# Optimization experiments

Hardware: AMD Instinct MI355X
Metric: run time of the kernel (lower is better)

## Reference

```python
import jax, jax.numpy as jnp
import numpy as np

B, IN_DIM, OUT_DIM, N, H = 64, 2, 1, 512, 64
SEQ, HOR, K, NSUP = 12, 12, 2, 2
TOT = 1 + NSUP * K  # number of diffusion matrices (identity + K steps per support)


def _lin_init(key, fan_in, shape):
    return jax.random.normal(key, shape, jnp.float32) / np.sqrt(fan_in)


def setup_inputs() -> dict:
    key = jax.random.key(0)
    ks = jax.random.split(key, 16)
    inputs = jax.random.normal(ks[0], (B, IN_DIM, N, SEQ), jnp.float32)
    A = jax.random.uniform(ks[1], (NSUP, N, N), jnp.float32)
    supports = A / A.sum(axis=2, keepdims=True)  # row-normalized transition matrices
    params = {}
    i = 2
    for pre, in0 in (('e', IN_DIM), ('d', OUT_DIM)):
        for l in range(2):
            cin = (in0 if l == 0 else H) + H
            params[f'{pre}{l}_wg'] = _lin_init(ks[i], TOT * cin, (TOT * cin, 2 * H)); i += 1
            params[f'{pre}{l}_bg'] = jnp.zeros((2 * H,), jnp.float32)
            params[f'{pre}{l}_wc'] = _lin_init(ks[i], TOT * cin, (TOT * cin, H)); i += 1
            params[f'{pre}{l}_bc'] = jnp.zeros((H,), jnp.float32)
    params['proj_w'] = _lin_init(ks[i], H, (OUT_DIM, H))
    params['proj_b'] = jnp.zeros((OUT_DIM,), jnp.float32)
    return {'inputs': inputs, 'supports': supports, **params}


def _gconv(x, h, supports, W, b):
    # x: (B,Cx,N), h: (B,H,N) -> (B,Dout,N)
    z = jnp.concatenate([x, h], axis=1)
    feats = [z]
    for s in range(NSUP):
        xk = z
        for _ in range(K):
            xk = jnp.einsum('nm,bcm->bcn', supports[s], xk)
            feats.append(xk)
    zf = jnp.concatenate(feats, axis=1)  # (B, TOT*C, N)
    return jnp.einsum('bcn,cd->bdn', zf, W) + b[None, :, None]


def _cell(x, h, supports, wg, bg, wc, bc):
    ru = jax.nn.sigmoid(_gconv(x, h, supports, wg, bg))
    r, u = jnp.split(ru, 2, axis=1)
    c = jnp.tanh(_gconv(x, r * h, supports, wc, bc))
    return u * h + (1.0 - u) * c


def _run(inputs, supports, p):
    h0 = jnp.zeros((B, H, N), jnp.float32)
    h1 = jnp.zeros((B, H, N), jnp.float32)

    def enc_step(carry, x):
        h0, h1 = carry
        h0 = _cell(x, h0, supports, p['e0_wg'], p['e0_bg'], p['e0_wc'], p['e0_bc'])
        h1 = _cell(h0, h1, supports, p['e1_wg'], p['e1_bg'], p['e1_wc'], p['e1_bc'])
        return (h0, h1), None

    xs = jnp.moveaxis(inputs, -1, 0)  # (SEQ,B,IN_DIM,N)
    (h0, h1), _ = jax.lax.scan(enc_step, (h0, h1), xs)

    go = jnp.zeros((B, OUT_DIM, N), jnp.float32)

    def dec_step(carry, _):
        x, h0, h1 = carry
        h0 = _cell(x, h0, supports, p['d0_wg'], p['d0_bg'], p['d0_wc'], p['d0_bc'])
        h1 = _cell(h0, h1, supports, p['d1_wg'], p['d1_bg'], p['d1_wc'], p['d1_bc'])
        y = jnp.einsum('bhn,oh->bon', h1, p['proj_w']) + p['proj_b'][None, :, None]
        return (y, h0, h1), y

    _, ys = jax.lax.scan(dec_step, (go, h0, h1), None, length=HOR)
    return jnp.moveaxis(ys, 0, -1)  # (B, OUT_DIM, N, HOR)


def reference(inputs, supports, e0_wg, e0_bg, e0_wc, e0_bc, e1_wg, e1_bg, e1_wc, e1_bc,
              d0_wg, d0_bg, d0_wc, d0_bc, d1_wg, d1_bg, d1_wc, d1_bc, proj_w, proj_b):
    p = dict(e0_wg=e0_wg, e0_bg=e0_bg, e0_wc=e0_wc, e0_bc=e0_bc,
             e1_wg=e1_wg, e1_bg=e1_bg, e1_wc=e1_wc, e1_bc=e1_bc,
             d0_wg=d0_wg, d0_bg=d0_bg, d0_wc=d0_wc, d0_bc=d0_bc,
             d1_wg=d1_wg, d1_bg=d1_bg, d1_wc=d1_wc, d1_bc=d1_bc,
             proj_w=proj_w, proj_b=proj_b)
    return _run(inputs, supports, p)
```

## Files before the change

kernel.cpp:

```cpp
#include <hip/hip_runtime.h>

#define B_ 64
#define N_ 512

typedef __attribute__((ext_vector_type(8))) short bf8_t;
typedef __attribute__((ext_vector_type(16))) float f16_t;
typedef __attribute__((ext_vector_type(4))) float f4v_t;

#define MFMA32(a, b, c) __builtin_amdgcn_mfma_f32_32x32x16_bf16(a, b, c, 0, 0, 0)

__device__ __forceinline__ ushort f2bf(float x) {
  union { float f; unsigned u; } v; v.f = x;
  unsigned r = v.u + 0x7FFFu + ((v.u >> 16) & 1u);
  return (ushort)(r >> 16);
}
__device__ __forceinline__ float bf2f(ushort h) {
  union { unsigned u; float f; } v; v.u = ((unsigned)h) << 16;
  return v.f;
}

__device__ __forceinline__ void gld16(const ushort* g, ushort* l) {
  __builtin_amdgcn_global_load_lds(
      (const __attribute__((address_space(1))) unsigned int*)(uintptr_t)g,
      (__attribute__((address_space(3))) unsigned int*)(uintptr_t)l,
      16, 0, 0);
}

__device__ __forceinline__ int xcd_logical(int nwg) {
  int lin = blockIdx.x + gridDim.x * (blockIdx.y + gridDim.y * blockIdx.z);
  return (lin & 7) * (nwg >> 3) + (lin >> 3);
}

__device__ __forceinline__ int swz32(int r) { return (r >> 1) & 3; }

template <int ROWS, int THREADS>
__device__ __forceinline__ void stage_tile2(const ushort* g, int lda, int k0,
                                            ushort* l, int tid) {
  constexpr int RT = (ROWS * 32) / (THREADS * 8);
#pragma unroll
  for (int q = 0; q < RT; ++q) {
    int e  = q * THREADS * 8 + tid * 8;
    int r  = e >> 5;
    int c8 = (e >> 3) & 3;
    int g8 = c8 ^ swz32(r);
    gld16(g + (size_t)r * lda + k0 + g8 * 8, l + e);
  }
}

__device__ __forceinline__ void core128(
    const ushort* Ah, const ushort* Al, int lda,
    const ushort* Bh, const ushort* Bl, int ldb,
    int K, ushort* lds, f16_t acc[2][2]) {
  constexpr int TILE = 128 * 32;
  constexpr int SSZ  = 4 * TILE;
  const int tid = threadIdx.x, lane = tid & 63, wave = tid >> 6;
  const int ar = lane & 31, hb = lane >> 5;
  const int wm = wave >> 1, wn = wave & 1;

  auto stage = [&](int buf, int k0) {
    ushort* lb = lds + buf * SSZ;
    stage_tile2<128, 256>(Ah, lda, k0, lb, tid);
    stage_tile2<128, 256>(Al, lda, k0, lb + TILE, tid);
    stage_tile2<128, 256>(Bh, ldb, k0, lb + 2 * TILE, tid);
    stage_tile2<128, 256>(Bl, ldb, k0, lb + 3 * TILE, tid);
  };

  const int nc = K >> 5;
  stage(0, 0);
  int buf = 0;
  for (int c = 0; c < nc; ++c) {
    __syncthreads();
    if (c + 1 < nc) stage(buf ^ 1, (c + 1) << 5);
    const ushort* lb = lds + buf * SSZ;
#pragma unroll
    for (int ks = 0; ks < 2; ++ks) {
      bf8_t ah[2], al[2], bh[2], bl[2];
#pragma unroll
      for (int i = 0; i < 2; ++i) {
        int r = wm * 64 + 32 * i + ar;
        int c8 = (ks * 2 + hb) ^ swz32(r);
        ah[i] = *(const bf8_t*)(lb + r * 32 + c8 * 8);
        al[i] = *(const bf8_t*)(lb + TILE + r * 32 + c8 * 8);
      }
#pragma unroll
      for (int j = 0; j < 2; ++j) {
        int r = wn * 64 + 32 * j + ar;
        int c8 = (ks * 2 + hb) ^ swz32(r);
        bh[j] = *(const bf8_t*)(lb + 2 * TILE + r * 32 + c8 * 8);
        bl[j] = *(const bf8_t*)(lb + 3 * TILE + r * 32 + c8 * 8);
      }
#pragma unroll
      for (int i = 0; i < 2; ++i)
#pragma unroll
        for (int j = 0; j < 2; ++j) {
          acc[i][j] = MFMA32(ah[i], bh[j], acc[i][j]);
          acc[i][j] = MFMA32(ah[i], bl[j], acc[i][j]);
          acc[i][j] = MFMA32(al[i], bh[j], acc[i][j]);
        }
    }
    buf ^= 1;
  }
}

__device__ __forceinline__ void core128_1(
    const ushort* Ah, int lda,
    const ushort* Bh, int ldb,
    int K, ushort* lds, f16_t acc[2][2]) {
  constexpr int TILE = 128 * 32;
  constexpr int SSZ  = 2 * TILE;
  const int tid = threadIdx.x, lane = tid & 63, wave = tid >> 6;
  const int ar = lane & 31, hb = lane >> 5;
  const int wm = wave >> 1, wn = wave & 1;

  auto stage = [&](int buf, int k0) {
    ushort* lb = lds + buf * SSZ;
    stage_tile2<128, 256>(Ah, lda, k0, lb, tid);
    stage_tile2<128, 256>(Bh, ldb, k0, lb + TILE, tid);
  };

  const int nc = K >> 5;
  stage(0, 0);
  int buf = 0;
  for (int c = 0; c < nc; ++c) {
    __syncthreads();
    if (c + 1 < nc) stage(buf ^ 1, (c + 1) << 5);
    const ushort* lb = lds + buf * SSZ;
#pragma unroll
    for (int ks = 0; ks < 2; ++ks) {
      bf8_t ah[2], bh[2];
#pragma unroll
      for (int i = 0; i < 2; ++i) {
        int r = wm * 64 + 32 * i + ar;
        int c8 = (ks * 2 + hb) ^ swz32(r);
        ah[i] = *(const bf8_t*)(lb + r * 32 + c8 * 8);
      }
#pragma unroll
      for (int j = 0; j < 2; ++j) {
        int r = wn * 64 + 32 * j + ar;
        int c8 = (ks * 2 + hb) ^ swz32(r);
        bh[j] = *(const bf8_t*)(lb + TILE + r * 32 + c8 * 8);
      }
#pragma unroll
      for (int i = 0; i < 2; ++i)
#pragma unroll
        for (int j = 0; j < 2; ++j)
          acc[i][j] = MFMA32(ah[i], bh[j], acc[i][j]);
    }
    buf ^= 1;
  }
}

__device__ __forceinline__ int crow32(int r, int hb) {
  return (r & 3) + 8 * (r >> 2) + 4 * hb;
}

__global__ __launch_bounds__(256) void ssq_k(const float* __restrict__ S,
                                             float* __restrict__ SS) {
  int s = blockIdx.z;
  const float* Ss = S + s * N_ * N_;
  __shared__ float Ta[16][17], Tb[16][17];
  int n = blockIdx.y * 16 + threadIdx.y;
  int m = blockIdx.x * 16 + threadIdx.x;
  float acc = 0.f;
  for (int p0 = 0; p0 < N_; p0 += 16) {
    Ta[threadIdx.y][threadIdx.x] = Ss[n * N_ + p0 + threadIdx.x];
    Tb[threadIdx.y][threadIdx.x] = Ss[(p0 + threadIdx.y) * N_ + m];
    __syncthreads();
#pragma unroll
    for (int pp = 0; pp < 16; ++pp)
      acc = fmaf(Ta[threadIdx.y][pp], Tb[pp][threadIdx.x], acc);
    __syncthreads();
  }
  SS[((size_t)s * N_ + n) * N_ + m] = acc;
}

__global__ __launch_bounds__(256) void bcat_k(const float* __restrict__ S,
                                              const float* __restrict__ SS,
                                              ushort* __restrict__ Bh) {
  int idx = blockIdx.x * 256 + threadIdx.x;
  if (idx >= 512 * 2048) return;
  int k = idx & 2047, n = idx >> 11;
  int seg = k >> 9, m = k & 511;
  float v;
  if (seg == 0)      v = S[(size_t)n * 512 + m];
  else if (seg == 1) v = SS[(size_t)n * 512 + m];
  else if (seg == 2) v = S[(size_t)(512 + n) * 512 + m];
  else               v = SS[(size_t)(512 + n) * 512 + m];
  Bh[idx] = f2bf(v);
}

__global__ __launch_bounds__(256) void wprep_id_k(const float* __restrict__ W,
                                                  ushort* __restrict__ Wh,
                                                  ushort* __restrict__ Wl,
                                                  int C, int Dout) {
  int idx = blockIdx.x * 256 + threadIdx.x;
  if (idx >= Dout * 128) return;
  int c = idx & 127, d = idx >> 7;
  float v = (c < C) ? W[(size_t)c * Dout + d] : 0.f;
  ushort hh = f2bf(v);
  Wh[idx] = hh; Wl[idx] = f2bf(v - bf2f(hh));
}

__global__ __launch_bounds__(256) void wprep_diff_k(const float* __restrict__ W,
                                                    ushort* __restrict__ Wh,
                                                    int C, int Dout) {
  int idx = blockIdx.x * 256 + threadIdx.x;
  if (idx >= 4 * Dout * 128) return;
  int c = idx & 127, i = idx >> 7;
  int t = 1 + i / Dout, d = i % Dout;
  float v = (c < C) ? W[(size_t)(t * C + c) * Dout + d] : 0.f;
  Wh[idx] = f2bf(v);
}

__global__ __launch_bounds__(256) void packzT_k(const float* __restrict__ xsrc,
                                                int xmode, int t, int Cx, int C,
                                                const float* __restrict__ hT,
                                                ushort* __restrict__ Zh,
                                                ushort* __restrict__ Zl) {
  int jg = blockIdx.x * 256 + threadIdx.x;
  int b = jg >> 9, n = jg & 511;
  for (int c0 = 0; c0 < 128; c0 += 8) {
    bf8_t vh, vl;
#pragma unroll
    for (int q = 0; q < 8; ++q) {
      int c = c0 + q;
      float v;
      if (c < Cx) {
        if (xmode == 0)      v = xsrc[((size_t)(b * Cx + c) * 512 + n) * 12 + t];
        else if (xmode == 1) v = xsrc[jg];
        else                 v = xsrc[(size_t)jg * 64 + c];
      } else if (c < C) {
        v = hT[(size_t)jg * 64 + (c - Cx)];
      } else {
        v = 0.f;
      }
      ushort hh = f2bf(v);
      vh[q] = (short)hh;
      vl[q] = (short)f2bf(v - bf2f(hh));
    }
    *(bf8_t*)(Zh + (size_t)jg * 128 + c0) = vh;
    *(bf8_t*)(Zl + (size_t)jg * 128 + c0) = vl;
  }
}

template <int MODE>
__global__ __launch_bounds__(256, 2) void g1id_k(const ushort* __restrict__ Wh,
                                                 const ushort* __restrict__ Wl,
                                                 const ushort* __restrict__ Zh,
                                                 const ushort* __restrict__ Zl,
                                                 float* __restrict__ G0T, int K) {
  __shared__ __attribute__((aligned(16))) ushort lds[2 * 4 * 128 * 32];
  constexpr int DR = (MODE == 0) ? 128 : 64;
  int tid = threadIdx.x, lane = tid & 63, wave = tid >> 6;
  int wm = wave >> 1, wn = wave & 1, ar = lane & 31, hb = lane >> 5;
  int nt = xcd_logical(256);
  f16_t acc[2][2] = {};
  core128(Wh, Wl, 128,
          Zh + (size_t)nt * 128 * 128, Zl + (size_t)nt * 128 * 128, 128,
          K, lds, acc);
#pragma unroll
  for (int i = 0; i < 2; ++i)
#pragma unroll
    for (int j = 0; j < 2; ++j) {
      int jg = nt * 128 + wn * 64 + 32 * j + ar;
#pragma unroll
      for (int r = 0; r < 16; ++r) {
        int d = wm * 64 + 32 * i + crow32(r, hb);
        if (d >= DR) continue;
        G0T[(size_t)jg * DR + d] = acc[i][j][r];
      }
    }
}

template <int MODE>
__global__ __launch_bounds__(256, 3) void g1diff_k(const ushort* __restrict__ Wd,
                                                   const ushort* __restrict__ Zh,
                                                   ushort* __restrict__ Gh, int K) {
  __shared__ __attribute__((aligned(16))) ushort lds[2 * 2 * 128 * 32];
  constexpr int DR = (MODE == 0) ? 128 : 64;
  constexpr int NMT = (MODE == 0) ? 4 : 2;
  int tid = threadIdx.x, lane = tid & 63, wave = tid >> 6;
  int wm = wave >> 1, wn = wave & 1, ar = lane & 31, hb = lane >> 5;
  int L = xcd_logical(256 * NMT);
  int mt = L % NMT, nt = L / NMT;
  f16_t acc[2][2] = {};
  core128_1(Wd + (size_t)mt * 128 * 128, 128,
            Zh + (size_t)nt * 128 * 128, 128,
            K, lds, acc);
#pragma unroll
  for (int i = 0; i < 2; ++i)
#pragma unroll
    for (int j = 0; j < 2; ++j) {
      int jg = nt * 128 + wn * 64 + 32 * j + ar;
      int b = jg >> 9, m = jg & 511;
#pragma unroll
      for (int r = 0; r < 16; ++r) {
        int ii = mt * 128 + wm * 64 + 32 * i + crow32(r, hb);
        int tt = ii / DR, d = ii % DR;
        Gh[((size_t)(b * DR + d)) * 2048 + (size_t)tt * 512 + m] = f2bf(acc[i][j][r]);
      }
    }
}

__global__ __launch_bounds__(256, 3) void ru1g_k(const ushort* __restrict__ Gh,
                                                 const ushort* __restrict__ Bch,
                                                 float* __restrict__ P) {
  __shared__ __attribute__((aligned(16))) ushort lds[2 * 2 * 128 * 32];
  int tid = threadIdx.x, lane = tid & 63, wave = tid >> 6;
  int wm = wave >> 1, wn = wave & 1, ar = lane & 31, hb = lane >> 5;
  int L = xcd_logical(768);
  int mt = L & 3, nt = (L >> 2) & 63, kz = L >> 8;
  int k0 = kz * 768;
  int K  = (kz == 2) ? 512 : 768;
  f16_t acc[2][2] = {};
  core128_1(Bch + (size_t)mt * 128 * 2048 + k0, 2048,
            Gh + (size_t)nt * 128 * 2048 + k0, 2048,
            K, lds, acc);
  float* Pz = P + (size_t)kz * 4194304;
#pragma unroll
  for (int i = 0; i < 2; ++i)
#pragma unroll
    for (int j = 0; j < 2; ++j) {
      int R = nt * 128 + wn * 64 + 32 * j + ar;
      int b = R >> 7, d = R & 127;
#pragma unroll
      for (int r = 0; r < 16; ++r) {
        int node = mt * 128 + wm * 64 + 32 * i + crow32(r, hb);
        Pz[((size_t)b * 512 + node) * 128 + d] = acc[i][j][r];
      }
    }
}

__global__ __launch_bounds__(256) void ru1f_k(const float* __restrict__ P,
                                              const float* __restrict__ G0T,
                                              const float* __restrict__ bg,
                                              const float* __restrict__ hT,
                                              float* __restrict__ U,
                                              ushort* __restrict__ Zh,
                                              ushort* __restrict__ Zl, int Cx) {
  int i4 = blockIdx.x * 256 + threadIdx.x;
  if (i4 >= 1048576) return;
  int base = i4 * 4;
  int row = base >> 7, d = base & 127;
  f4v_t p0 = *(const f4v_t*)(P + base);
  f4v_t p1 = *(const f4v_t*)(P + 4194304 + base);
  f4v_t p2 = *(const f4v_t*)(P + 2 * 4194304 + base);
  f4v_t g0 = *(const f4v_t*)(G0T + base);
  if (d < 64) {
    f4v_t hv = *(const f4v_t*)(hT + (size_t)row * 64 + d);
#pragma unroll
    for (int e = 0; e < 4; ++e) {
      float s = 1.f / (1.f + expf(-(p0[e] + p1[e] + p2[e] + g0[e] + bg[d + e])));
      float rh = s * hv[e];
      ushort hh = f2bf(rh);
      Zh[(size_t)row * 128 + Cx + d + e] = hh;
      Zl[(size_t)row * 128 + Cx + d + e] = f2bf(rh - bf2f(hh));
    }
  } else {
    f4v_t uo;
#pragma unroll
    for (int e = 0; e < 4; ++e)
      uo[e] = 1.f / (1.f + expf(-(p0[e] + p1[e] + p2[e] + g0[e] + bg[d + e])));
    *(f4v_t*)(U + (size_t)row * 64 + (d - 64)) = uo;
  }
}

__global__ __launch_bounds__(256, 3) void ru2g_k(const ushort* __restrict__ Gh,
                                                 const ushort* __restrict__ Bch,
                                                 float* __restrict__ P) {
  __shared__ __attribute__((aligned(16))) ushort lds[2 * 2 * 128 * 32];
  int tid = threadIdx.x, lane = tid & 63, wave = tid >> 6;
  int wm = wave >> 1, wn = wave & 1, ar = lane & 31, hb = lane >> 5;
  int L = xcd_logical(512);
  int mt = L & 3, nt = (L >> 2) & 31, kz = L >> 7;
  f16_t acc[2][2] = {};
  core128_1(Bch + (size_t)mt * 128 * 2048 + kz * 512, 2048,
            Gh + (size_t)nt * 128 * 2048 + kz * 512, 2048,
            512, lds, acc);
  float* Pz = P + (size_t)kz * 2097152;
#pragma unroll
  for (int i = 0; i < 2; ++i)
#pragma unroll
    for (int j = 0; j < 2; ++j) {
      int R = nt * 128 + wn * 64 + 32 * j + ar;
      int b = R >> 6, d = R & 63;
#pragma unroll
      for (int r = 0; r < 16; ++r) {
        int node = mt * 128 + wm * 64 + 32 * i + crow32(r, hb);
        Pz[((size_t)b * 512 + node) * 64 + d] = acc[i][j][r];
      }
    }
}

__global__ __launch_bounds__(256) void ru2f_k(const float* __restrict__ P,
                                              const float* __restrict__ G0c,
                                              const float* __restrict__ bc,
                                              const float* __restrict__ U,
                                              float* __restrict__ hT) {
  int i4 = blockIdx.x * 256 + threadIdx.x;
  if (i4 >= 524288) return;
  int base = i4 * 4;
  int d = base & 63;
  f4v_t p0 = *(const f4v_t*)(P + base);
  f4v_t p1 = *(const f4v_t*)(P + 2097152 + base);
  f4v_t p2 = *(const f4v_t*)(P + 2 * 2097152 + base);
  f4v_t p3 = *(const f4v_t*)(P + 3 * 2097152 + base);
  f4v_t g0 = *(const f4v_t*)(G0c + base);
  f4v_t uv = *(const f4v_t*)(U + base);
  f4v_t hv = *(const f4v_t*)(hT + base);
#pragma unroll
  for (int e = 0; e < 4; ++e) {
    float ct = tanhf(p0[e] + p1[e] + p2[e] + p3[e] + g0[e] + bc[d + e]);
    hv[e] = uv[e] * hv[e] + (1.f - uv[e]) * ct;
  }
  *(f4v_t*)(hT + base) = hv;
}

__global__ __launch_bounds__(256) void proj_out_k(const float* __restrict__ h1T,
                                                  const float* __restrict__ pw,
                                                  const float* __restrict__ pb,
                                                  float* __restrict__ ybuf,
                                                  float* __restrict__ out, int k) {
  int idx = blockIdx.x * blockDim.x + threadIdx.x;
  if (idx >= B_ * N_) return;
  float s = pb[0];
  const float* hrow = h1T + (size_t)idx * 64;
#pragma unroll
  for (int j = 0; j < 64; ++j)
    s = fmaf(pw[j], hrow[j], s);
  ybuf[idx] = s;
  out[(size_t)idx * 12 + k] = s;
}

extern "C" void kernel_launch(void* const* d_in, const int* in_sizes, int n_in,
                              void* d_out, int out_size, void* d_ws, size_t ws_size,
                              hipStream_t stream) {
  const float* inputs   = (const float*)d_in[0];
  const float* supports = (const float*)d_in[1];
  const float* Wg[4] = { (const float*)d_in[2],  (const float*)d_in[6],
                         (const float*)d_in[10], (const float*)d_in[14] };
  const float* Bg[4] = { (const float*)d_in[3],  (const float*)d_in[7],
                         (const float*)d_in[11], (const float*)d_in[15] };
  const float* Wc[4] = { (const float*)d_in[4],  (const float*)d_in[8],
                         (const float*)d_in[12], (const float*)d_in[16] };
  const float* Bc[4] = { (const float*)d_in[5],  (const float*)d_in[9],
                         (const float*)d_in[13], (const float*)d_in[17] };
  const float* proj_w = (const float*)d_in[18];
  const float* proj_b = (const float*)d_in[19];
  float* out = (float*)d_out;

  char* p = (char*)d_ws;
  auto carve = [&](size_t bytes) { void* q = p; p += (bytes + 255) & ~(size_t)255; return q; };
  ushort* Bch = (ushort*)carve((size_t)512 * 2048 * 2);
  ushort* zTh = (ushort*)carve((size_t)32768 * 128 * 2);
  ushort* zTl = (ushort*)carve((size_t)32768 * 128 * 2);
  ushort* Gh  = (ushort*)carve((size_t)8192 * 2048 * 2);
  float*  G0T = (float*)carve((size_t)32768 * 128 * 4);
  float*  P   = (float*)carve((size_t)3 * 4194304 * 4);
  float*  U   = (float*)carve((size_t)2097152 * 4);
  float*  h0  = (float*)carve((size_t)2097152 * 4);
  float*  h1  = (float*)carve((size_t)2097152 * 4);
  float*  ybuf = (float*)carve((size_t)B_ * N_ * 4);
  ushort* Wgid_h[4]; ushort* Wgid_l[4]; ushort* Wgd[4];
  ushort* Wcid_h[4]; ushort* Wcid_l[4]; ushort* Wcd[4];
  for (int c = 0; c < 4; ++c) {
    Wgid_h[c] = (ushort*)carve((size_t)128 * 128 * 2);
    Wgid_l[c] = (ushort*)carve((size_t)128 * 128 * 2);
    Wgd[c]    = (ushort*)carve((size_t)512 * 128 * 2);
    Wcid_h[c] = (ushort*)carve((size_t)64 * 128 * 2);
    Wcid_l[c] = (ushort*)carve((size_t)64 * 128 * 2);
    Wcd[c]    = (ushort*)carve((size_t)256 * 128 * 2);
  }
  float* SSbuf = (float*)U;

  hipMemsetAsync(h0, 0, (size_t)2097152 * 4, stream);
  hipMemsetAsync(h1, 0, (size_t)2097152 * 4, stream);
  hipMemsetAsync(ybuf, 0, (size_t)B_ * N_ * 4, stream);

  ssq_k<<<dim3(32, 32, 2), dim3(16, 16), 0, stream>>>(supports, SSbuf);
  bcat_k<<<(512 * 2048 + 255) / 256, 256, 0, stream>>>(supports, SSbuf, Bch);
  const int Cs[4] = { 66, 128, 65, 128 };
  for (int c = 0; c < 4; ++c) {
    wprep_id_k<<<(128 * 128 + 255) / 256, 256, 0, stream>>>(Wg[c], Wgid_h[c], Wgid_l[c], Cs[c], 128);
    wprep_diff_k<<<(4 * 128 * 128 + 255) / 256, 256, 0, stream>>>(Wg[c], Wgd[c], Cs[c], 128);
    wprep_id_k<<<(64 * 128 + 255) / 256, 256, 0, stream>>>(Wc[c], Wcid_h[c], Wcid_l[c], Cs[c], 64);
    wprep_diff_k<<<(4 * 64 * 128 + 255) / 256, 256, 0, stream>>>(Wc[c], Wcd[c], Cs[c], 64);
  }

  auto cell = [&](int ci, int Cx, const float* x, int xmode, int t, float* h) {
    int C = Cx + 64;
    int K1 = (C + 31) & ~31;
    packzT_k<<<128, 256, 0, stream>>>(x, xmode, t, Cx, C, h, zTh, zTl);
    g1id_k<0><<<256, 256, 0, stream>>>(Wgid_h[ci], Wgid_l[ci], zTh, zTl, G0T, K1);
    g1diff_k<0><<<dim3(256, 4), 256, 0, stream>>>(Wgd[ci], zTh, Gh, K1);
    ru1g_k<<<dim3(64, 4, 3), 256, 0, stream>>>(Gh, Bch, P);
    ru1f_k<<<4096, 256, 0, stream>>>(P, G0T, Bg[ci], h, U, zTh, zTl, Cx);
    g1id_k<1><<<256, 256, 0, stream>>>(Wcid_h[ci], Wcid_l[ci], zTh, zTl, G0T, K1);
    g1diff_k<1><<<dim3(256, 2), 256, 0, stream>>>(Wcd[ci], zTh, Gh, K1);
    ru2g_k<<<dim3(32, 4, 4), 256, 0, stream>>>(Gh, Bch, P);
    ru2f_k<<<2048, 256, 0, stream>>>(P, G0T, Bc[ci], U, h);
  };

  for (int t = 0; t < 12; ++t) {
    cell(0, 2, inputs, 0, t, h0);
    cell(1, 64, h0, 2, 0, h1);
  }
  for (int k = 0; k < 12; ++k) {
    cell(2, 1, ybuf, 1, 0, h0);
    cell(3, 64, h0, 2, 0, h1);
    proj_out_k<<<(B_ * N_ + 255) / 256, 256, 0, stream>>>(h1, proj_w, proj_b, ybuf, out, k);
  }
}
```

Before: 6.450 ms.

## Merge identity and diffusion weight GEMMs into one launch and batch setup kernels

The separate identity-term (hi/lo split) and diffusion-term weight GEMM kernels are merged into a single g1_k launch, where an extra grid slice handles the identity product. This removes two launches per cell (96 in total) and lets both GEMMs share the GPU concurrently. Setup is also reworked: the S² precompute now uses a bf16 MFMA GEMM on a transposed copy instead of a scalar fp32 kernel, the sixteen weight-prep kernels become one, and the three memsets become one. The fused kernel uses the larger LDS footprint and occupancy bound of the identity path for all blocks, and S² is now computed from bf16 inputs, which may slightly change accuracy.

```diff
diff --git a/kernel.cpp b/kernel.cpp
--- a/kernel.cpp
+++ b/kernel.cpp
@@ -154,62 +154,75 @@
   return (r & 3) + 8 * (r >> 2) + 4 * hb;
 }
 
-__global__ __launch_bounds__(256) void ssq_k(const float* __restrict__ S,
-                                             float* __restrict__ SS) {
+__global__ __launch_bounds__(256) void stb_k(const float* __restrict__ S,
+                                             ushort* __restrict__ Bcat,
+                                             ushort* __restrict__ STb) {
+  __shared__ float tile[16][17];
   int s = blockIdx.z;
-  const float* Ss = S + s * N_ * N_;
-  __shared__ float Ta[16][17], Tb[16][17];
-  int n = blockIdx.y * 16 + threadIdx.y;
-  int m = blockIdx.x * 16 + threadIdx.x;
-  float acc = 0.f;
-  for (int p0 = 0; p0 < N_; p0 += 16) {
-    Ta[threadIdx.y][threadIdx.x] = Ss[n * N_ + p0 + threadIdx.x];
-    Tb[threadIdx.y][threadIdx.x] = Ss[(p0 + threadIdx.y) * N_ + m];
-    __syncthreads();
-#pragma unroll
-    for (int pp = 0; pp < 16; ++pp)
-      acc = fmaf(Ta[threadIdx.y][pp], Tb[pp][threadIdx.x], acc);
-    __syncthreads();
-  }
-  SS[((size_t)s * N_ + n) * N_ + m] = acc;
-}
-
-__global__ __launch_bounds__(256) void bcat_k(const float* __restrict__ S,
-                                              const float* __restrict__ SS,
-                                              ushort* __restrict__ Bh) {
+  int n0 = blockIdx.y * 16, m0 = blockIdx.x * 16;
+  int tx = threadIdx.x & 15, ty = threadIdx.x >> 4;
+  float v = S[(size_t)s * 262144 + (size_t)(n0 + ty) * 512 + m0 + tx];
+  tile[ty][tx] = v;
+  Bcat[(size_t)(n0 + ty) * 2048 + (size_t)(2 * s) * 512 + m0 + tx] = f2bf(v);
+  __syncthreads();
+  STb[(size_t)s * 262144 + (size_t)(m0 + ty) * 512 + n0 + tx] = f2bf(tile[tx][ty]);
+}
+
+__global__ __launch_bounds__(256) void ssqm_k(const ushort* __restrict__ Bc,
+                                              const ushort* __restrict__ STb,
+                                              ushort* __restrict__ Bout) {
+  __shared__ __attribute__((aligned(16))) ushort lds[2 * 2 * 128 * 32];
+  int tid = threadIdx.x, lane = tid & 63, wave = tid >> 6;
+  int wm = wave >> 1, wn = wave & 1, ar = lane & 31, hb = lane >> 5;
+  int a = blockIdx.x, bm = blockIdx.y, s = blockIdx.z;
+  f16_t acc[2][2] = {};
+  core128_1(Bc + (size_t)(a * 128) * 2048 + (size_t)(2 * s) * 512, 2048,
+            STb + (size_t)s * 262144 + (size_t)(bm * 128) * 512, 512,
+            512, lds, acc);
+#pragma unroll
+  for (int i = 0; i < 2; ++i)
+#pragma unroll
+    for (int j = 0; j < 2; ++j) {
+      int m_ = bm * 128 + wn * 64 + 32 * j + ar;
+#pragma unroll
+      for (int r = 0; r < 16; ++r) {
+        int n_ = a * 128 + wm * 64 + 32 * i + crow32(r, hb);
+        Bout[(size_t)n_ * 2048 + (size_t)(2 * s + 1) * 512 + m_] = f2bf(acc[i][j][r]);
+      }
+    }
+}
+
+struct WSrc { const float* wg[4]; const float* wc[4]; };
+
+__global__ __launch_bounds__(256) void wprep_all_k(WSrc src,
+                                                   ushort* __restrict__ Wbuf) {
   int idx = blockIdx.x * 256 + threadIdx.x;
-  if (idx >= 512 * 2048) return;
-  int k = idx & 2047, n = idx >> 11;
-  int seg = k >> 9, m = k & 511;
-  float v;
-  if (seg == 0)      v = S[(size_t)n * 512 + m];
-  else if (seg == 1) v = SS[(size_t)n * 512 + m];
-  else if (seg == 2) v = S[(size_t)(512 + n) * 512 + m];
-  else               v = SS[(size_t)(512 + n) * 512 + m];
-  Bh[idx] = f2bf(v);
-}
-
-__global__ __launch_bounds__(256) void wprep_id_k(const float* __restrict__ W,
-                                                  ushort* __restrict__ Wh,
-                                                  ushort* __restrict__ Wl,
-                                                  int C, int Dout) {
-  int idx = blockIdx.x * 256 + threadIdx.x;
-  if (idx >= Dout * 128) return;
-  int c = idx & 127, d = idx >> 7;
-  float v = (c < C) ? W[(size_t)c * Dout + d] : 0.f;
-  ushort hh = f2bf(v);
-  Wh[idx] = hh; Wl[idx] = f2bf(v - bf2f(hh));
-}
-
-__global__ __launch_bounds__(256) void wprep_diff_k(const float* __restrict__ W,
-                                                    ushort* __restrict__ Wh,
-                                                    int C, int Dout) {
-  int idx = blockIdx.x * 256 + threadIdx.x;
-  if (idx >= 4 * Dout * 128) return;
-  int c = idx & 127, i = idx >> 7;
-  int t = 1 + i / Dout, d = i % Dout;
-  float v = (c < C) ? W[(size_t)(t * C + c) * Dout + d] : 0.f;
-  Wh[idx] = f2bf(v);
+  if (idx >= 4 * 147456) return;
+  int ci = idx / 147456, r = idx % 147456;
+  int C = (ci == 0) ? 66 : (ci == 2) ? 65 : 128;
+  const float* WG = src.wg[ci];
+  const float* WC = src.wc[ci];
+  ushort v;
+  if (r < 32768) {
+    int e = r & 16383, c = e & 127, d = e >> 7;
+    float x = (c < C) ? WG[(size_t)c * 128 + d] : 0.f;
+    ushort hh = f2bf(x);
+    v = (r < 16384) ? hh : f2bf(x - bf2f(hh));
+  } else if (r < 98304) {
+    int e = r - 32768, c = e & 127, i = e >> 7;
+    int t = 1 + (i >> 7), d = i & 127;
+    v = (c < C) ? f2bf(WG[(size_t)(t * C + c) * 128 + d]) : (ushort)0;
+  } else if (r < 114688) {
+    int e = (r - 98304) & 8191, c = e & 127, d = e >> 7;
+    float x = (c < C) ? WC[(size_t)c * 64 + d] : 0.f;
+    ushort hh = f2bf(x);
+    v = (r < 106496) ? hh : f2bf(x - bf2f(hh));
+  } else {
+    int e = r - 114688, c = e & 127, i = e >> 7;
+    int t = 1 + (i >> 6), d = i & 63;
+    v = (c < C) ? f2bf(WC[(size_t)(t * C + c) * 64 + d]) : (ushort)0;
+  }
+  Wbuf[idx] = v;
 }
 
 __global__ __launch_bounds__(256) void packzT_k(const float* __restrict__ xsrc,
@@ -244,62 +257,55 @@
 }
 
 template <int MODE>
-__global__ __launch_bounds__(256, 2) void g1id_k(const ushort* __restrict__ Wh,
-                                                 const ushort* __restrict__ Wl,
-                                                 const ushort* __restrict__ Zh,
-                                                 const ushort* __restrict__ Zl,
-                                                 float* __restrict__ G0T, int K) {
+__global__ __launch_bounds__(256, 2) void g1_k(const ushort* __restrict__ Wih,
+                                               const ushort* __restrict__ Wil,
+                                               const ushort* __restrict__ Wd,
+                                               const ushort* __restrict__ Zh,
+                                               const ushort* __restrict__ Zl,
+                                               ushort* __restrict__ Gh,
+                                               float* __restrict__ G0T, int K) {
   __shared__ __attribute__((aligned(16))) ushort lds[2 * 4 * 128 * 32];
-  constexpr int DR = (MODE == 0) ? 128 : 64;
-  int tid = threadIdx.x, lane = tid & 63, wave = tid >> 6;
-  int wm = wave >> 1, wn = wave & 1, ar = lane & 31, hb = lane >> 5;
-  int nt = xcd_logical(256);
-  f16_t acc[2][2] = {};
-  core128(Wh, Wl, 128,
-          Zh + (size_t)nt * 128 * 128, Zl + (size_t)nt * 128 * 128, 128,
-          K, lds, acc);
-#pragma unroll
-  for (int i = 0; i < 2; ++i)
-#pragma unroll
-    for (int j = 0; j < 2; ++j) {
-      int jg = nt * 128 + wn * 64 + 32 * j + ar;
-#pragma unroll
-      for (int r = 0; r < 16; ++r) {
-        int d = wm * 64 + 32 * i + crow32(r, hb);
-        if (d >= DR) continue;
-        G0T[(size_t)jg * DR + d] = acc[i][j][r];
-      }
-    }
-}
-
-template <int MODE>
-__global__ __launch_bounds__(256, 3) void g1diff_k(const ushort* __restrict__ Wd,
-                                                   const ushort* __restrict__ Zh,
-                                                   ushort* __restrict__ Gh, int K) {
-  __shared__ __attribute__((aligned(16))) ushort lds[2 * 2 * 128 * 32];
   constexpr int DR = (MODE == 0) ? 128 : 64;
   constexpr int NMT = (MODE == 0) ? 4 : 2;
   int tid = threadIdx.x, lane = tid & 63, wave = tid >> 6;
   int wm = wave >> 1, wn = wave & 1, ar = lane & 31, hb = lane >> 5;
-  int L = xcd_logical(256 * NMT);
-  int mt = L % NMT, nt = L / NMT;
+  int L = xcd_logical(256 * (NMT + 1));
+  int mt = L % (NMT + 1), nt = L / (NMT + 1);
   f16_t acc[2][2] = {};
-  core128_1(Wd + (size_t)mt * 128 * 128, 128,
-            Zh + (size_t)nt * 128 * 128, 128,
+  if (mt == NMT) {
+    core128(Wih, Wil, 128,
+            Zh + (size_t)nt * 128 * 128, Zl + (size_t)nt * 128 * 128, 128,
             K, lds, acc);
 #pragma unroll
-  for (int i = 0; i < 2; ++i)
-#pragma unroll
-    for (int j = 0; j < 2; ++j) {
-      int jg = nt * 128 + wn * 64 + 32 * j + ar;
-      int b = jg >> 9, m = jg & 511;
-#pragma unroll
-      for (int r = 0; r < 16; ++r) {
-        int ii = mt * 128 + wm * 64 + 32 * i + crow32(r, hb);
-        int tt = ii / DR, d = ii % DR;
-        Gh[((size_t)(b * DR + d)) * 2048 + (size_t)tt * 512 + m] = f2bf(acc[i][j][r]);
-      }
-    }
+    for (int i = 0; i < 2; ++i)
+#pragma unroll
+      for (int j = 0; j < 2; ++j) {
+        int jg = nt * 128 + wn * 64 + 32 * j + ar;
+#pragma unroll
+        for (int r = 0; r < 16; ++r) {
+          int d = wm * 64 + 32 * i + crow32(r, hb);
+          if (d >= DR) continue;
+          G0T[(size_t)jg * DR + d] = acc[i][j][r];
+        }
+      }
+  } else {
+    core128_1(Wd + (size_t)mt * 128 * 128, 128,
+              Zh + (size_t)nt * 128 * 128, 128,
+              K, lds, acc);
+#pragma unroll
+    for (int i = 0; i < 2; ++i)
+#pragma unroll
+      for (int j = 0; j < 2; ++j) {
+        int jg = nt * 128 + wn * 64 + 32 * j + ar;
+        int b = jg >> 9, m = jg & 511;
+#pragma unroll
+        for (int r = 0; r < 16; ++r) {
+          int ii = mt * 128 + wm * 64 + 32 * i + crow32(r, hb);
+          int tt = ii / DR, d = ii % DR;
+          Gh[((size_t)(b * DR + d)) * 2048 + (size_t)tt * 512 + m] = f2bf(acc[i][j][r]);
+        }
+      }
+  }
 }
 
 __global__ __launch_bounds__(256, 3) void ru1g_k(const ushort* __restrict__ Gh,
@@ -437,12 +443,13 @@
                               hipStream_t stream) {
   const float* inputs   = (const float*)d_in[0];
   const float* supports = (const float*)d_in[1];
-  const float* Wg[4] = { (const float*)d_in[2],  (const float*)d_in[6],
-                         (const float*)d_in[10], (const float*)d_in[14] };
+  WSrc wsrc;
+  wsrc.wg[0] = (const float*)d_in[2];  wsrc.wg[1] = (const float*)d_in[6];
+  wsrc.wg[2] = (const float*)d_in[10]; wsrc.wg[3] = (const float*)d_in[14];
+  wsrc.wc[0] = (const float*)d_in[4];  wsrc.wc[1] = (const float*)d_in[8];
+  wsrc.wc[2] = (const float*)d_in[12]; wsrc.wc[3] = (const float*)d_in[16];
   const float* Bg[4] = { (const float*)d_in[3],  (const float*)d_in[7],
                          (const float*)d_in[11], (const float*)d_in[15] };
-  const float* Wc[4] = { (const float*)d_in[4],  (const float*)d_in[8],
-                         (const float*)d_in[12], (const float*)d_in[16] };
   const float* Bc[4] = { (const float*)d_in[5],  (const float*)d_in[9],
                          (const float*)d_in[13], (const float*)d_in[17] };
   const float* proj_w = (const float*)d_in[18];
@@ -451,52 +458,38 @@
 
   char* p = (char*)d_ws;
   auto carve = [&](size_t bytes) { void* q = p; p += (bytes + 255) & ~(size_t)255; return q; };
-  ushort* Bch = (ushort*)carve((size_t)512 * 2048 * 2);
-  ushort* zTh = (ushort*)carve((size_t)32768 * 128 * 2);
-  ushort* zTl = (ushort*)carve((size_t)32768 * 128 * 2);
-  ushort* Gh  = (ushort*)carve((size_t)8192 * 2048 * 2);
-  float*  G0T = (float*)carve((size_t)32768 * 128 * 4);
-  float*  P   = (float*)carve((size_t)3 * 4194304 * 4);
-  float*  U   = (float*)carve((size_t)2097152 * 4);
-  float*  h0  = (float*)carve((size_t)2097152 * 4);
-  float*  h1  = (float*)carve((size_t)2097152 * 4);
+  ushort* Bch  = (ushort*)carve((size_t)512 * 2048 * 2);
+  ushort* zTh  = (ushort*)carve((size_t)32768 * 128 * 2);
+  ushort* zTl  = (ushort*)carve((size_t)32768 * 128 * 2);
+  ushort* Gh   = (ushort*)carve((size_t)8192 * 2048 * 2);
+  float*  G0T  = (float*)carve((size_t)32768 * 128 * 4);
+  float*  P    = (float*)carve((size_t)3 * 4194304 * 4);
+  float*  U    = (float*)carve((size_t)2097152 * 4);
+  float*  h0   = (float*)carve((size_t)2097152 * 4);
+  float*  h1   = (float*)carve((size_t)2097152 * 4);
   float*  ybuf = (float*)carve((size_t)B_ * N_ * 4);
-  ushort* Wgid_h[4]; ushort* Wgid_l[4]; ushort* Wgd[4];
-  ushort* Wcid_h[4]; ushort* Wcid_l[4]; ushort* Wcd[4];
-  for (int c = 0; c < 4; ++c) {
-    Wgid_h[c] = (ushort*)carve((size_t)128 * 128 * 2);
-    Wgid_l[c] = (ushort*)carve((size_t)128 * 128 * 2);
-    Wgd[c]    = (ushort*)carve((size_t)512 * 128 * 2);
-    Wcid_h[c] = (ushort*)carve((size_t)64 * 128 * 2);
-    Wcid_l[c] = (ushort*)carve((size_t)64 * 128 * 2);
-    Wcd[c]    = (ushort*)carve((size_t)256 * 128 * 2);
-  }
-  float* SSbuf = (float*)U;
-
-  hipMemsetAsync(h0, 0, (size_t)2097152 * 4, stream);
-  hipMemsetAsync(h1, 0, (size_t)2097152 * 4, stream);
-  hipMemsetAsync(ybuf, 0, (size_t)B_ * N_ * 4, stream);
-
-  ssq_k<<<dim3(32, 32, 2), dim3(16, 16), 0, stream>>>(supports, SSbuf);
-  bcat_k<<<(512 * 2048 + 255) / 256, 256, 0, stream>>>(supports, SSbuf, Bch);
-  const int Cs[4] = { 66, 128, 65, 128 };
-  for (int c = 0; c < 4; ++c) {
-    wprep_id_k<<<(128 * 128 + 255) / 256, 256, 0, stream>>>(Wg[c], Wgid_h[c], Wgid_l[c], Cs[c], 128);
-    wprep_diff_k<<<(4 * 128 * 128 + 255) / 256, 256, 0, stream>>>(Wg[c], Wgd[c], Cs[c], 128);
-    wprep_id_k<<<(64 * 128 + 255) / 256, 256, 0, stream>>>(Wc[c], Wcid_h[c], Wcid_l[c], Cs[c], 64);
-    wprep_diff_k<<<(4 * 64 * 128 + 255) / 256, 256, 0, stream>>>(Wc[c], Wcd[c], Cs[c], 64);
-  }
+  ushort* Wbuf = (ushort*)carve((size_t)4 * 147456 * 2);
+  ushort* STb  = (ushort*)U;
+
+  hipMemsetAsync(h0, 0, (size_t)2097152 * 4 * 2 + (size_t)B_ * N_ * 4, stream);
+
+  stb_k<<<dim3(32, 32, 2), 256, 0, stream>>>(supports, Bch, STb);
+  ssqm_k<<<dim3(4, 4, 2), 256, 0, stream>>>(Bch, STb, Bch);
+  wprep_all_k<<<(4 * 147456 + 255) / 256, 256, 0, stream>>>(wsrc, Wbuf);
 
   auto cell = [&](int ci, int Cx, const float* x, int xmode, int t, float* h) {
     int C = Cx + 64;
     int K1 = (C + 31) & ~31;
+    ushort* cw = Wbuf + (size_t)ci * 147456;
+    ushort* Wgid_h = cw;          ushort* Wgid_l = cw + 16384;
+    ushort* Wgd    = cw + 32768;
+    ushort* Wcid_h = cw + 98304;  ushort* Wcid_l = cw + 106496;
+    ushort* Wcd    = cw + 114688;
     packzT_k<<<128, 256, 0, stream>>>(x, xmode, t, Cx, C, h, zTh, zTl);
-    g1id_k<0><<<256, 256, 0, stream>>>(Wgid_h[ci], Wgid_l[ci], zTh, zTl, G0T, K1);
-    g1diff_k<0><<<dim3(256, 4), 256, 0, stream>>>(Wgd[ci], zTh, Gh, K1);
+    g1_k<0><<<dim3(256, 5), 256, 0, stream>>>(Wgid_h, Wgid_l, Wgd, zTh, zTl, Gh, G0T, K1);
     ru1g_k<<<dim3(64, 4, 3), 256, 0, stream>>>(Gh, Bch, P);
     ru1f_k<<<4096, 256, 0, stream>>>(P, G0T, Bg[ci], h, U, zTh, zTl, Cx);
-    g1id_k<1><<<256, 256, 0, stream>>>(Wcid_h[ci], Wcid_l[ci], zTh, zTl, G0T, K1);
-    g1diff_k<1><<<dim3(256, 2), 256, 0, stream>>>(Wcd[ci], zTh, Gh, K1);
+    g1_k<1><<<dim3(256, 3), 256, 0, stream>>>(Wcid_h, Wcid_l, Wcd, zTh, zTl, Gh, G0T, K1);
     ru2g_k<<<dim3(32, 4, 4), 256, 0, stream>>>(Gh, Bch, P);
     ru2f_k<<<2048, 256, 0, stream>>>(P, G0T, Bc[ci], U, h);
   };
```

Result: faster. 6.206 ms (-3.8%).
